# Performance work log

Measured on AMD Instinct MI355X. Metric: run time of the kernel, lower is better.

The kernel has to match this reference:

```python
import jax, jax.numpy as jnp
import numpy as np

N = 50000      # nodes
E = 1600000    # edges (avg degree 32)
F_IN = 128     # num_features
DIM = 64       # hidden dim
L = 3          # num_gc_layers
G = 500        # graphs in batch


def setup_inputs() -> dict:
    key = jax.random.key(0)
    ks = jax.random.split(key, 16)
    inp = {}
    inp["x"] = jax.random.normal(ks[0], (N, F_IN), dtype=jnp.float32)
    inp["edge_index"] = jax.random.randint(ks[1], (2, E), 0, N, dtype=jnp.int32)
    inp["batch"] = jnp.sort(jax.random.randint(ks[2], (N,), 0, G, dtype=jnp.int32))
    # GIN layer MLP params: layer0 maps F_IN->DIM->DIM, later layers DIM->DIM->DIM
    d_in = F_IN
    ki = 3
    for i in range(L):
        inp[f"W1_{i}"] = jax.random.normal(ks[ki], (d_in, DIM), dtype=jnp.float32) / np.sqrt(d_in); ki += 1
        inp[f"b1_{i}"] = jnp.zeros((DIM,), dtype=jnp.float32)
        inp[f"W2_{i}"] = jax.random.normal(ks[ki], (DIM, DIM), dtype=jnp.float32) / np.sqrt(DIM); ki += 1
        inp[f"b2_{i}"] = jnp.zeros((DIM,), dtype=jnp.float32)
        d_in = DIM
    # final scoring head: concat readout -> dim * L inputs, 1 output
    inp["Wm"] = jax.random.normal(ks[ki], (DIM * L, 1), dtype=jnp.float32) / np.sqrt(DIM * L)
    inp["bm"] = jnp.zeros((1,), dtype=jnp.float32)
    return inp


def _segment_softmax(scores, seg, num_segments):
    # numerically stable softmax over elements grouped by seg; scores [M, 1]
    m = jax.ops.segment_max(scores, seg, num_segments=num_segments)
    e = jnp.exp(scores - m[seg])
    denom = jax.ops.segment_sum(e, seg, num_segments=num_segments)
    return e / denom[seg]


def _forward(x, edge_index, batch, params):
    src, dst = edge_index[0], edge_index[1]
    n = x.shape[0]
    xs = []
    h = x
    for i in range(L):
        W1, b1, W2, b2 = params[4 * i: 4 * i + 4]
        # GINConv (eps=0): h_i <- MLP(h_i + sum_{j->i} h_j)
        agg = jax.ops.segment_sum(h[src], dst, num_segments=n)
        h = jax.nn.relu((h + agg) @ W1 + b1) @ W2 + b2
        if i != L - 1:
            h = jax.nn.relu(h)
        xs.append(h)
    node_prob = jnp.concatenate(xs, axis=1)            # concat readout [N, DIM*L]
    Wm, bm = params[4 * L], params[4 * L + 1]
    node_score = node_prob @ Wm + bm                   # [N, 1]
    # lift_node_score_to_edge_score
    src_score = node_score[src]                        # [E, 1]
    dst_score = node_score[dst]
    edge_score = src_score * dst_score
    edge_prop = _segment_softmax(edge_score, dst, n)   # softmax over edges per dst
    new_score = jax.ops.segment_sum(src_score * edge_prop, dst, num_segments=n)
    node_score = node_score + new_score
    # final softmax over nodes grouped by graph id
    return _segment_softmax(node_score, batch, G)


def reference(x, edge_index, batch, W1_0, b1_0, W2_0, b2_0, W1_1, b1_1, W2_1, b2_1,
              W1_2, b1_2, W2_2, b2_2, Wm, bm):
    params = [W1_0, b1_0, W2_0, b2_0, W1_1, b1_1, W2_1, b2_1,
              W1_2, b1_2, W2_2, b2_2, Wm, bm]
    return _forward(x, edge_index, batch, params)
```

## Files before the change

kernel.cpp:

```cpp
#include <hip/hip_runtime.h>
#include <math.h>

#define N_NODES 50000
#define N_EDGES 1600000
#define N_GRAPH 500
#define CHUNKS 64
#define EPC (N_EDGES / CHUNKS)

__device__ __forceinline__ float rl(float v, int k) {
    return __int_as_float(__builtin_amdgcn_readlane(__float_as_int(v), k));
}

__global__ __launch_bounds__(1024) void histsort_kernel(const int* __restrict__ src,
                                                        const int* __restrict__ dst,
                                                        int* __restrict__ csrc_chunk,
                                                        unsigned* __restrict__ cntloc,
                                                        unsigned short* __restrict__ lr_g) {
    __shared__ unsigned packed[N_NODES / 2];
    __shared__ unsigned aux[1024];
    const int c = blockIdx.x;
    const int s0 = c * EPC;
    const int tid = threadIdx.x;

    for (int i = tid; i < N_NODES / 2; i += 1024) packed[i] = 0;
    __syncthreads();

    for (int e = s0 + tid; e < s0 + EPC; e += 1024) {
        int d = dst[e];
        int sh = (d & 1) * 16;
        unsigned old = atomicAdd(&packed[d >> 1], 1u << sh);
        lr_g[e] = (unsigned short)((old >> sh) & 0xffffu);
    }
    __syncthreads();

    const int W = 25;
    int w0 = tid * W;
    int w1 = min(w0 + W, N_NODES / 2);
    unsigned run = 0;
    for (int i = w0; i < w1; i++) {
        unsigned v = packed[i];
        unsigned lo = v & 0xffffu, hi = v >> 16;
        packed[i] = run | ((run + lo) << 16);
        run += lo + hi;
    }
    aux[tid] = run;
    __syncthreads();
    for (int off = 1; off < 1024; off <<= 1) {
        unsigned t = (tid >= off) ? aux[tid - off] : 0;
        __syncthreads();
        aux[tid] += t;
        __syncthreads();
    }
    unsigned b0 = (tid == 0) ? 0 : aux[tid - 1];
    if (b0) {
        unsigned addv = b0 | (b0 << 16);
        for (int i = w0; i < w1; i++) packed[i] += addv;
    }
    __syncthreads();

    int* outc = csrc_chunk + (size_t)c * EPC;
    for (int e = s0 + tid; e < s0 + EPC; e += 1024) {
        int d = dst[e];
        unsigned pw = packed[d >> 1];
        unsigned loc = (d & 1) ? (pw >> 16) : (pw & 0xffffu);
        outc[loc + lr_g[e]] = src[e];
    }
    unsigned* clc = cntloc + (size_t)c * N_NODES;
    for (int d = tid; d < N_NODES; d += 1024) {
        unsigned pw = packed[d >> 1];
        unsigned loc = (d & 1) ? (pw >> 16) : (pw & 0xffffu);
        unsigned nxt;
        if (d + 1 < N_NODES) {
            unsigned pw2 = packed[(d + 1) >> 1];
            nxt = ((d + 1) & 1) ? (pw2 >> 16) : (pw2 & 0xffffu);
        } else {
            nxt = EPC;
        }
        clc[d] = ((nxt - loc) << 16) | loc;
    }
}

__global__ __launch_bounds__(1024) void base_scan1_kernel(const unsigned* __restrict__ cntloc,
                                                          unsigned short* __restrict__ base,
                                                          int* __restrict__ deg,
                                                          int* __restrict__ part, int N) {
    int d = blockIdx.x * 1024 + threadIdx.x;
    int run = 0;
    if (d < N) {
#pragma unroll 8
        for (int c = 0; c < CHUNKS; c++) {
            int v = (int)(cntloc[(size_t)c * N + d] >> 16);
            base[(size_t)c * N + d] = (unsigned short)run;
            run += v;
        }
        deg[d] = run;
    }
    int v = run;
#pragma unroll
    for (int o = 32; o >= 1; o >>= 1) v += __shfl_xor(v, o);
    __shared__ int red[16];
    if ((threadIdx.x & 63) == 0) red[threadIdx.x >> 6] = v;
    __syncthreads();
    if (threadIdx.x == 0) {
        int s = 0;
#pragma unroll
        for (int k = 0; k < 16; k++) s += red[k];
        part[blockIdx.x] = s;
    }
}

__global__ void scan2_kernel(int* __restrict__ part, int nb) {
    int lane = threadIdx.x;
    int v = (lane < nb) ? part[lane] : 0;
    int orig = v;
#pragma unroll
    for (int o = 1; o < 64; o <<= 1) {
        int t = __shfl_up(v, o);
        if (lane >= o) v += t;
    }
    if (lane < nb) part[lane] = v - orig;
    if (lane == nb - 1) part[nb] = v;
}

__global__ __launch_bounds__(1024) void scan3_kernel(const int* __restrict__ deg,
                                                     const int* __restrict__ part,
                                                     int* __restrict__ rowptr, int N) {
    int i = blockIdx.x * 1024 + threadIdx.x;
    int lane = threadIdx.x & 63;
    int w = threadIdx.x >> 6;
    int v = (i < N) ? deg[i] : 0;
    int inc = v;
#pragma unroll
    for (int o = 1; o < 64; o <<= 1) {
        int t = __shfl_up(inc, o);
        if (lane >= o) inc += t;
    }
    __shared__ int wsum[16];
    if (lane == 63) wsum[w] = inc;
    __syncthreads();
    if (threadIdx.x < 16) {
        int x = wsum[threadIdx.x];
        int xo = x;
#pragma unroll
        for (int o = 1; o < 16; o <<= 1) {
            int t = __shfl_up(x, o);
            if ((int)threadIdx.x >= o) x += t;
        }
        wsum[threadIdx.x] = x - xo;
    }
    __syncthreads();
    int b = part[blockIdx.x] + wsum[w];
    if (i < N) {
        rowptr[i] = b + inc - v;
        if (i == N - 1) rowptr[N] = b + inc;
    }
}

__global__ __launch_bounds__(256) void gatherfill_kernel(const int* __restrict__ csrc_chunk,
                                                         const unsigned* __restrict__ cntloc,
                                                         const unsigned short* __restrict__ base,
                                                         const int* __restrict__ rowptr,
                                                         int* __restrict__ csr_src) {
    const int perXcd = N_NODES / 8;
    int xcd = blockIdx.x & 7;
    int idx = (blockIdx.x >> 3) * 4 + ((threadIdx.x) >> 6);
    if (idx >= perXcd) return;
    int wid = xcd * perXcd + idx;
    int lane = threadIdx.x & 63;
    unsigned cl = cntloc[(size_t)lane * N_NODES + wid];
    int cnt = (int)(cl >> 16);
    int loc = (int)(cl & 0xffffu);
    int ob = rowptr[wid] + (int)base[(size_t)lane * N_NODES + wid];
    const int* in = csrc_chunk + (size_t)lane * EPC + loc;
    for (int i = 0; i < cnt; i++) csr_src[ob + i] = in[i];
}

__global__ __launch_bounds__(256) void agg_kernel(const float* __restrict__ y,
                                                  const int* __restrict__ rowptr,
                                                  const int* __restrict__ csr_src,
                                                  float* __restrict__ u, int N) {
    int wid = (blockIdx.x * 256 + threadIdx.x) >> 6;
    int lane = threadIdx.x & 63;
    if (wid >= N) return;
    int q = lane >> 4;
    int r = lane & 15;
    int start = rowptr[wid];
    int end = rowptr[wid + 1];
    float4 acc = make_float4(0.f, 0.f, 0.f, 0.f);
    int j = start;
    for (; j + 32 <= end; j += 32) {
        int s0 = csr_src[j + q];
        int s1 = csr_src[j + 4 + q];
        int s2 = csr_src[j + 8 + q];
        int s3 = csr_src[j + 12 + q];
        int s4 = csr_src[j + 16 + q];
        int s5 = csr_src[j + 20 + q];
        int s6 = csr_src[j + 24 + q];
        int s7 = csr_src[j + 28 + q];
        float4 v0 = *(const float4*)(y + (size_t)s0 * 64 + r * 4);
        float4 v1 = *(const float4*)(y + (size_t)s1 * 64 + r * 4);
        float4 v2 = *(const float4*)(y + (size_t)s2 * 64 + r * 4);
        float4 v3 = *(const float4*)(y + (size_t)s3 * 64 + r * 4);
        float4 v4 = *(const float4*)(y + (size_t)s4 * 64 + r * 4);
        float4 v5 = *(const float4*)(y + (size_t)s5 * 64 + r * 4);
        float4 v6 = *(const float4*)(y + (size_t)s6 * 64 + r * 4);
        float4 v7 = *(const float4*)(y + (size_t)s7 * 64 + r * 4);
        acc.x += ((v0.x + v1.x) + (v2.x + v3.x)) + ((v4.x + v5.x) + (v6.x + v7.x));
        acc.y += ((v0.y + v1.y) + (v2.y + v3.y)) + ((v4.y + v5.y) + (v6.y + v7.y));
        acc.z += ((v0.z + v1.z) + (v2.z + v3.z)) + ((v4.z + v5.z) + (v6.z + v7.z));
        acc.w += ((v0.w + v1.w) + (v2.w + v3.w)) + ((v4.w + v5.w) + (v6.w + v7.w));
    }
#pragma unroll
    for (int m = 0; m < 8; m++) {
        int e = j + 4 * m + q;
        if (e < end) {
            int s = csr_src[e];
            float4 v = *(const float4*)(y + (size_t)s * 64 + r * 4);
            acc.x += v.x; acc.y += v.y; acc.z += v.z; acc.w += v.w;
        }
    }
    acc.x += __shfl_xor(acc.x, 16);
    acc.y += __shfl_xor(acc.y, 16);
    acc.z += __shfl_xor(acc.z, 16);
    acc.w += __shfl_xor(acc.w, 16);
    acc.x += __shfl_xor(acc.x, 32);
    acc.y += __shfl_xor(acc.y, 32);
    acc.z += __shfl_xor(acc.z, 32);
    acc.w += __shfl_xor(acc.w, 32);
    if (lane < 16) {
        float4 self = *(const float4*)(y + (size_t)wid * 64 + r * 4);
        acc.x += self.x; acc.y += self.y; acc.z += self.z; acc.w += self.w;
        *(float4*)(u + (size_t)wid * 64 + r * 4) = acc;
    }
}

__global__ __launch_bounds__(256) void gemm0_kernel(const float* __restrict__ x,
                                                    const float* __restrict__ W1,
                                                    float* __restrict__ y0,
                                                    int N, int totalWaves) {
    int lane = threadIdx.x & 63;
    int wid = (blockIdx.x * 256 + threadIdx.x) >> 6;
    float w[64];
#pragma unroll
    for (int k = 0; k < 64; k++) w[k] = W1[k * 64 + lane];
    for (int node = wid; node < N; node += totalWaves) {
        float xa = x[node * 128 + lane];
        float a0 = 0.f, a1 = 0.f, a2 = 0.f, a3 = 0.f;
#pragma unroll
        for (int k = 0; k < 64; k += 4) {
            a0 = fmaf(rl(xa, k + 0), w[k + 0], a0);
            a1 = fmaf(rl(xa, k + 1), w[k + 1], a1);
            a2 = fmaf(rl(xa, k + 2), w[k + 2], a2);
            a3 = fmaf(rl(xa, k + 3), w[k + 3], a3);
        }
        y0[node * 64 + lane] = (a0 + a1) + (a2 + a3);
    }
#pragma unroll
    for (int k = 0; k < 64; k++) w[k] = W1[(64 + k) * 64 + lane];
    for (int node = wid; node < N; node += totalWaves) {
        float xb = x[node * 128 + 64 + lane];
        float a0 = 0.f, a1 = 0.f, a2 = 0.f, a3 = 0.f;
#pragma unroll
        for (int k = 0; k < 64; k += 4) {
            a0 = fmaf(rl(xb, k + 0), w[k + 0], a0);
            a1 = fmaf(rl(xb, k + 1), w[k + 1], a1);
            a2 = fmaf(rl(xb, k + 2), w[k + 2], a2);
            a3 = fmaf(rl(xb, k + 3), w[k + 3], a3);
        }
        y0[node * 64 + lane] += (a0 + a1) + (a2 + a3);
    }
}

template <int LAYER>
__global__ __launch_bounds__(256) void mlpAB_kernel(const float* __restrict__ u,
                                                    const float* __restrict__ b1,
                                                    const float* __restrict__ W2,
                                                    const float* __restrict__ b2,
                                                    const float* __restrict__ W1n,
                                                    const float* __restrict__ Wm,
                                                    float* __restrict__ ynext,
                                                    float* __restrict__ score,
                                                    int N, int totalWaves) {
    int lane = threadIdx.x & 63;
    int wid = (blockIdx.x * 256 + threadIdx.x) >> 6;
    float w2[64], w1[64];
#pragma unroll
    for (int k = 0; k < 64; k++) w2[k] = W2[k * 64 + lane];
#pragma unroll
    for (int k = 0; k < 64; k++) w1[k] = W1n[k * 64 + lane];
    float bb1 = b1[lane], bb2 = b2[lane], wm = Wm[LAYER * 64 + lane];

    int node = wid;
    float uin = (node < N) ? u[node * 64 + lane] : 0.f;
    for (; node < N; node += totalWaves) {
        int nn = node + totalWaves;
        float unext = (nn < N) ? u[nn * 64 + lane] : 0.f;
        float t = fmaxf(uin + bb1, 0.f);
        float a0 = 0.f, a1 = 0.f, a2 = 0.f, a3 = 0.f;
#pragma unroll
        for (int k = 0; k < 64; k += 4) {
            a0 = fmaf(rl(t, k + 0), w2[k + 0], a0);
            a1 = fmaf(rl(t, k + 1), w2[k + 1], a1);
            a2 = fmaf(rl(t, k + 2), w2[k + 2], a2);
            a3 = fmaf(rl(t, k + 3), w2[k + 3], a3);
        }
        float h = fmaxf(bb2 + ((a0 + a1) + (a2 + a3)), 0.f);
        float p = h * wm;
#pragma unroll
        for (int o = 32; o >= 1; o >>= 1) p += __shfl_xor(p, o);
        if (lane == 0) {
            if (LAYER == 0) score[node] = p;
            else score[node] += p;
        }
        float y0 = 0.f, y1 = 0.f, y2 = 0.f, y3 = 0.f;
#pragma unroll
        for (int k = 0; k < 64; k += 4) {
            y0 = fmaf(rl(h, k + 0), w1[k + 0], y0);
            y1 = fmaf(rl(h, k + 1), w1[k + 1], y1);
            y2 = fmaf(rl(h, k + 2), w1[k + 2], y2);
            y3 = fmaf(rl(h, k + 3), w1[k + 3], y3);
        }
        ynext[node * 64 + lane] = (y0 + y1) + (y2 + y3);
        uin = unext;
    }
}

__global__ __launch_bounds__(256) void mlpA2_kernel(const float* __restrict__ u,
                                                    const float* __restrict__ b1,
                                                    const float* __restrict__ W2,
                                                    const float* __restrict__ b2,
                                                    const float* __restrict__ Wm,
                                                    float* __restrict__ score,
                                                    int N, int totalWaves) {
    int lane = threadIdx.x & 63;
    int wid = (blockIdx.x * 256 + threadIdx.x) >> 6;
    float w2[64];
#pragma unroll
    for (int k = 0; k < 64; k++) w2[k] = W2[k * 64 + lane];
    float bb1 = b1[lane], bb2 = b2[lane], wm = Wm[2 * 64 + lane];

    int node = wid;
    float uin = (node < N) ? u[node * 64 + lane] : 0.f;
    for (; node < N; node += totalWaves) {
        int nn = node + totalWaves;
        float unext = (nn < N) ? u[nn * 64 + lane] : 0.f;
        float t = fmaxf(uin + bb1, 0.f);
        float a0 = 0.f, a1 = 0.f, a2 = 0.f, a3 = 0.f;
#pragma unroll
        for (int k = 0; k < 64; k += 4) {
            a0 = fmaf(rl(t, k + 0), w2[k + 0], a0);
            a1 = fmaf(rl(t, k + 1), w2[k + 1], a1);
            a2 = fmaf(rl(t, k + 2), w2[k + 2], a2);
            a3 = fmaf(rl(t, k + 3), w2[k + 3], a3);
        }
        float h = bb2 + ((a0 + a1) + (a2 + a3));
        float p = h * wm;
#pragma unroll
        for (int o = 32; o >= 1; o >>= 1) p += __shfl_xor(p, o);
        if (lane == 0) score[node] += p;
        uin = unext;
    }
}

__global__ __launch_bounds__(256) void edge_softmax_kernel(const float* __restrict__ score,
                                                           const int* __restrict__ rowptr,
                                                           const int* __restrict__ csr_src,
                                                           const float* __restrict__ bm,
                                                           float* __restrict__ nsf, int N) {
    int wid = (blockIdx.x * blockDim.x + threadIdx.x) >> 6;
    int lane = threadIdx.x & 63;
    if (wid >= N) return;
    float b = bm[0];
    float sd = score[wid] + b;
    int start = rowptr[wid];
    int end = rowptr[wid + 1];
    bool has0 = (start + lane < end);
    float ss0 = 0.f;
    float m = -INFINITY;
    if (has0) {
        ss0 = score[csr_src[start + lane]] + b;
        m = ss0 * sd;
    }
    for (int j = start + 64 + lane; j < end; j += 64) {
        float ss = score[csr_src[j]] + b;
        m = fmaxf(m, ss * sd);
    }
#pragma unroll
    for (int o = 32; o >= 1; o >>= 1) m = fmaxf(m, __shfl_xor(m, o));
    float se = 0.f, swe = 0.f;
    if (m > -INFINITY) {
        if (has0) {
            float e0 = expf(ss0 * sd - m);
            se += e0;
            swe += ss0 * e0;
        }
        for (int j = start + 64 + lane; j < end; j += 64) {
            float ss = score[csr_src[j]] + b;
            float e = expf(ss * sd - m);
            se += e;
            swe += ss * e;
        }
#pragma unroll
        for (int o = 32; o >= 1; o >>= 1) {
            se += __shfl_xor(se, o);
            swe += __shfl_xor(swe, o);
        }
    }
    float ns = (se > 0.f) ? (swe / se) : 0.f;
    if (lane == 0) nsf[wid] = sd + ns;
}

__global__ __launch_bounds__(256) void graph_softmax_kernel(const float* __restrict__ nsf,
                                                            const int* __restrict__ batch,
                                                            float* __restrict__ out, int N) {
    int g = blockIdx.x;
    int tid = threadIdx.x;
    int lo = 0, hi = N;
    while (lo < hi) { int mid = (lo + hi) >> 1; if (batch[mid] < g) lo = mid + 1; else hi = mid; }
    int s0 = lo;
    hi = N;
    while (lo < hi) { int mid = (lo + hi) >> 1; if (batch[mid] < g + 1) lo = mid + 1; else hi = mid; }
    int s1 = lo;

    __shared__ float red[4];
    __shared__ float bval;
    float m = -INFINITY;
    for (int i = s0 + tid; i < s1; i += 256) m = fmaxf(m, nsf[i]);
#pragma unroll
    for (int o = 32; o >= 1; o >>= 1) m = fmaxf(m, __shfl_xor(m, o));
    if ((tid & 63) == 0) red[tid >> 6] = m;
    __syncthreads();
    if (tid == 0) bval = fmaxf(fmaxf(red[0], red[1]), fmaxf(red[2], red[3]));
    __syncthreads();
    float bmx = bval;
    float s = 0.f;
    for (int i = s0 + tid; i < s1; i += 256) {
        float e = expf(nsf[i] - bmx);
        out[i] = e;
        s += e;
    }
#pragma unroll
    for (int o = 32; o >= 1; o >>= 1) s += __shfl_xor(s, o);
    __syncthreads();
    if ((tid & 63) == 0) red[tid >> 6] = s;
    __syncthreads();
    if (tid == 0) bval = red[0] + red[1] + red[2] + red[3];
    __syncthreads();
    float inv = 1.f / bval;
    for (int i = s0 + tid; i < s1; i += 256) out[i] *= inv;
}

extern "C" void kernel_launch(void* const* d_in, const int* in_sizes, int n_in,
                              void* d_out, int out_size, void* d_ws, size_t ws_size,
                              hipStream_t stream) {
    const int N = N_NODES, E = N_EDGES;

    const float* x = (const float*)d_in[0];
    const int* ei = (const int*)d_in[1];
    const int* batch = (const int*)d_in[2];
    const float* W1a[3] = {(const float*)d_in[3], (const float*)d_in[7], (const float*)d_in[11]};
    const float* b1a[3] = {(const float*)d_in[4], (const float*)d_in[8], (const float*)d_in[12]};
    const float* W2a[3] = {(const float*)d_in[5], (const float*)d_in[9], (const float*)d_in[13]};
    const float* b2a[3] = {(const float*)d_in[6], (const float*)d_in[10], (const float*)d_in[14]};
    const float* Wm = (const float*)d_in[15];
    const float* bm = (const float*)d_in[16];
    float* out = (float*)d_out;

    const int* srcp = ei;
    const int* dstp = ei + E;

    float* yA = (float*)d_ws;
    float* yB = yA + (size_t)N * 64;
    float* ubuf = yB + (size_t)N * 64;
    int* csrc_chunk = (int*)ubuf;
    float* score = ubuf + (size_t)N * 64;
    float* nsf = score + N;
    int* deg = (int*)(nsf + N);
    int* rowptr = deg + N;
    int* part = rowptr + N + 1;
    int* csr_src = part + 64;
    unsigned* cntloc = (unsigned*)(csr_src + E);
    unsigned short* base = (unsigned short*)(cntloc + (size_t)CHUNKS * N);
    unsigned short* lr = base + (size_t)CHUNKS * N;

    histsort_kernel<<<CHUNKS, 1024, 0, stream>>>(srcp, dstp, csrc_chunk, cntloc, lr);

    const int nbScan = (N + 1023) / 1024;
    base_scan1_kernel<<<nbScan, 1024, 0, stream>>>(cntloc, base, deg, part, N);
    scan2_kernel<<<1, 64, 0, stream>>>(part, nbScan);
    scan3_kernel<<<nbScan, 1024, 0, stream>>>(deg, part, rowptr, N);

    const int gfBlocks = 8 * ((N / 8 + 3) / 4);
    gatherfill_kernel<<<gfBlocks, 256, 0, stream>>>(csrc_chunk, cntloc, base, rowptr, csr_src);

    const int gw = 4096;
    gemm0_kernel<<<1024, 256, 0, stream>>>(x, W1a[0], yA, N, gw);

    int aggBlocks = (N + 3) / 4;

    agg_kernel<<<aggBlocks, 256, 0, stream>>>(yA, rowptr, csr_src, ubuf, N);
    mlpAB_kernel<0><<<1024, 256, 0, stream>>>(ubuf, b1a[0], W2a[0], b2a[0], W1a[1], Wm, yB, score, N, gw);

    agg_kernel<<<aggBlocks, 256, 0, stream>>>(yB, rowptr, csr_src, ubuf, N);
    mlpAB_kernel<1><<<1024, 256, 0, stream>>>(ubuf, b1a[1], W2a[1], b2a[1], W1a[2], Wm, yA, score, N, gw);

    agg_kernel<<<aggBlocks, 256, 0, stream>>>(yA, rowptr, csr_src, ubuf, N);
    mlpA2_kernel<<<1024, 256, 0, stream>>>(ubuf, b1a[2], W2a[2], b2a[2], Wm, score, N, gw);

    edge_softmax_kernel<<<(N + 3) / 4, 256, 0, stream>>>(score, rowptr, csr_src, bm, nsf, N);

    graph_softmax_kernel<<<N_GRAPH, 256, 0, stream>>>(nsf, batch, out, N);
}
```

Measured before the change: 374.1 us.

## Store node features as fp16, double sort chunks, keep edge ranks in registers

Node feature buffers feeding the neighbour aggregation are now stored in half precision, which halves the bytes of the random gathers, and the sums are still accumulated in fp32. The histogram sort now uses 128 chunks instead of 64. It keeps per-edge local ranks in registers instead of a global array and stores only 16-bit chunk offsets, deriving counts from the difference of adjacent offsets. gemm0 now does both K-halves in one pass with 128 weight registers. The fp16 storage adds rounding error, and the register use in gemm0 may lower occupancy.

```diff
diff --git a/kernel.cpp b/kernel.cpp
--- a/kernel.cpp
+++ b/kernel.cpp
@@ -1,21 +1,30 @@
 #include <hip/hip_runtime.h>
+#include <hip/hip_fp16.h>
 #include <math.h>
 
 #define N_NODES 50000
 #define N_EDGES 1600000
 #define N_GRAPH 500
-#define CHUNKS 64
+#define CHUNKS 128
 #define EPC (N_EDGES / CHUNKS)
+#define NP1 (N_NODES + 1)
+#define NIT ((EPC + 1023) / 1024)
 
 __device__ __forceinline__ float rl(float v, int k) {
     return __int_as_float(__builtin_amdgcn_readlane(__float_as_int(v), k));
+}
+__device__ __forceinline__ void hacc(float4& a, uint2 w) {
+    __half2 h01 = *reinterpret_cast<__half2*>(&w.x);
+    __half2 h23 = *reinterpret_cast<__half2*>(&w.y);
+    float2 f01 = __half22float2(h01);
+    float2 f23 = __half22float2(h23);
+    a.x += f01.x; a.y += f01.y; a.z += f23.x; a.w += f23.y;
 }
 
 __global__ __launch_bounds__(1024) void histsort_kernel(const int* __restrict__ src,
                                                         const int* __restrict__ dst,
                                                         int* __restrict__ csrc_chunk,
-                                                        unsigned* __restrict__ cntloc,
-                                                        unsigned short* __restrict__ lr_g) {
+                                                        unsigned short* __restrict__ locs) {
     __shared__ unsigned packed[N_NODES / 2];
     __shared__ unsigned aux[1024];
     const int c = blockIdx.x;
@@ -25,11 +34,16 @@
     for (int i = tid; i < N_NODES / 2; i += 1024) packed[i] = 0;
     __syncthreads();
 
-    for (int e = s0 + tid; e < s0 + EPC; e += 1024) {
-        int d = dst[e];
-        int sh = (d & 1) * 16;
-        unsigned old = atomicAdd(&packed[d >> 1], 1u << sh);
-        lr_g[e] = (unsigned short)((old >> sh) & 0xffffu);
+    unsigned short lrv[NIT];
+#pragma unroll
+    for (int it = 0; it < NIT; it++) {
+        int e = s0 + it * 1024 + tid;
+        if (e < s0 + EPC) {
+            int d = dst[e];
+            int sh = (d & 1) * 16;
+            unsigned old = atomicAdd(&packed[d >> 1], 1u << sh);
+            lrv[it] = (unsigned short)((old >> sh) & 0xffffu);
+        }
     }
     __syncthreads();
 
@@ -59,28 +73,30 @@
     __syncthreads();
 
     int* outc = csrc_chunk + (size_t)c * EPC;
-    for (int e = s0 + tid; e < s0 + EPC; e += 1024) {
-        int d = dst[e];
-        unsigned pw = packed[d >> 1];
-        unsigned loc = (d & 1) ? (pw >> 16) : (pw & 0xffffu);
-        outc[loc + lr_g[e]] = src[e];
-    }
-    unsigned* clc = cntloc + (size_t)c * N_NODES;
-    for (int d = tid; d < N_NODES; d += 1024) {
-        unsigned pw = packed[d >> 1];
-        unsigned loc = (d & 1) ? (pw >> 16) : (pw & 0xffffu);
-        unsigned nxt;
-        if (d + 1 < N_NODES) {
-            unsigned pw2 = packed[(d + 1) >> 1];
-            nxt = ((d + 1) & 1) ? (pw2 >> 16) : (pw2 & 0xffffu);
+#pragma unroll
+    for (int it = 0; it < NIT; it++) {
+        int e = s0 + it * 1024 + tid;
+        if (e < s0 + EPC) {
+            int d = dst[e];
+            unsigned pw = packed[d >> 1];
+            unsigned loc = (d & 1) ? (pw >> 16) : (pw & 0xffffu);
+            outc[loc + lrv[it]] = src[e];
+        }
+    }
+    unsigned short* lc = locs + (size_t)c * NP1;
+    for (int d = tid; d <= N_NODES; d += 1024) {
+        unsigned short loc;
+        if (d == N_NODES) {
+            loc = (unsigned short)EPC;
         } else {
-            nxt = EPC;
-        }
-        clc[d] = ((nxt - loc) << 16) | loc;
-    }
-}
-
-__global__ __launch_bounds__(1024) void base_scan1_kernel(const unsigned* __restrict__ cntloc,
+            unsigned pw = packed[d >> 1];
+            loc = (unsigned short)((d & 1) ? (pw >> 16) : (pw & 0xffffu));
+        }
+        lc[d] = loc;
+    }
+}
+
+__global__ __launch_bounds__(1024) void base_scan1_kernel(const unsigned short* __restrict__ locs,
                                                           unsigned short* __restrict__ base,
                                                           int* __restrict__ deg,
                                                           int* __restrict__ part, int N) {
@@ -89,9 +105,10 @@
     if (d < N) {
 #pragma unroll 8
         for (int c = 0; c < CHUNKS; c++) {
-            int v = (int)(cntloc[(size_t)c * N + d] >> 16);
+            int l0 = locs[(size_t)c * NP1 + d];
+            int l1 = locs[(size_t)c * NP1 + d + 1];
             base[(size_t)c * N + d] = (unsigned short)run;
-            run += v;
+            run += l1 - l0;
         }
         deg[d] = run;
     }
@@ -157,25 +174,31 @@
 }
 
 __global__ __launch_bounds__(256) void gatherfill_kernel(const int* __restrict__ csrc_chunk,
-                                                         const unsigned* __restrict__ cntloc,
+                                                         const unsigned short* __restrict__ locs,
                                                          const unsigned short* __restrict__ base,
                                                          const int* __restrict__ rowptr,
                                                          int* __restrict__ csr_src) {
     const int perXcd = N_NODES / 8;
     int xcd = blockIdx.x & 7;
-    int idx = (blockIdx.x >> 3) * 4 + ((threadIdx.x) >> 6);
+    int idx = (blockIdx.x >> 3) * 4 + (threadIdx.x >> 6);
     if (idx >= perXcd) return;
     int wid = xcd * perXcd + idx;
     int lane = threadIdx.x & 63;
-    unsigned cl = cntloc[(size_t)lane * N_NODES + wid];
-    int cnt = (int)(cl >> 16);
-    int loc = (int)(cl & 0xffffu);
-    int ob = rowptr[wid] + (int)base[(size_t)lane * N_NODES + wid];
-    const int* in = csrc_chunk + (size_t)lane * EPC + loc;
-    for (int i = 0; i < cnt; i++) csr_src[ob + i] = in[i];
-}
-
-__global__ __launch_bounds__(256) void agg_kernel(const float* __restrict__ y,
+    int rp = rowptr[wid];
+#pragma unroll
+    for (int cc = 0; cc < 2; cc++) {
+        int c = lane + cc * 64;
+        const unsigned short* lc = locs + (size_t)c * NP1;
+        int l0 = lc[wid];
+        int l1 = lc[wid + 1];
+        int cnt = l1 - l0;
+        int ob = rp + (int)base[(size_t)c * N_NODES + wid];
+        const int* in = csrc_chunk + (size_t)c * EPC + l0;
+        for (int i = 0; i < cnt; i++) csr_src[ob + i] = in[i];
+    }
+}
+
+__global__ __launch_bounds__(256) void agg_kernel(const __half* __restrict__ yh,
                                                   const int* __restrict__ rowptr,
                                                   const int* __restrict__ csr_src,
                                                   float* __restrict__ u, int N) {
@@ -197,26 +220,24 @@
         int s5 = csr_src[j + 20 + q];
         int s6 = csr_src[j + 24 + q];
         int s7 = csr_src[j + 28 + q];
-        float4 v0 = *(const float4*)(y + (size_t)s0 * 64 + r * 4);
-        float4 v1 = *(const float4*)(y + (size_t)s1 * 64 + r * 4);
-        float4 v2 = *(const float4*)(y + (size_t)s2 * 64 + r * 4);
-        float4 v3 = *(const float4*)(y + (size_t)s3 * 64 + r * 4);
-        float4 v4 = *(const float4*)(y + (size_t)s4 * 64 + r * 4);
-        float4 v5 = *(const float4*)(y + (size_t)s5 * 64 + r * 4);
-        float4 v6 = *(const float4*)(y + (size_t)s6 * 64 + r * 4);
-        float4 v7 = *(const float4*)(y + (size_t)s7 * 64 + r * 4);
-        acc.x += ((v0.x + v1.x) + (v2.x + v3.x)) + ((v4.x + v5.x) + (v6.x + v7.x));
-        acc.y += ((v0.y + v1.y) + (v2.y + v3.y)) + ((v4.y + v5.y) + (v6.y + v7.y));
-        acc.z += ((v0.z + v1.z) + (v2.z + v3.z)) + ((v4.z + v5.z) + (v6.z + v7.z));
-        acc.w += ((v0.w + v1.w) + (v2.w + v3.w)) + ((v4.w + v5.w) + (v6.w + v7.w));
+        uint2 w0 = *(const uint2*)(yh + (size_t)s0 * 64 + r * 4);
+        uint2 w1 = *(const uint2*)(yh + (size_t)s1 * 64 + r * 4);
+        uint2 w2 = *(const uint2*)(yh + (size_t)s2 * 64 + r * 4);
+        uint2 w3 = *(const uint2*)(yh + (size_t)s3 * 64 + r * 4);
+        uint2 w4 = *(const uint2*)(yh + (size_t)s4 * 64 + r * 4);
+        uint2 w5 = *(const uint2*)(yh + (size_t)s5 * 64 + r * 4);
+        uint2 w6 = *(const uint2*)(yh + (size_t)s6 * 64 + r * 4);
+        uint2 w7 = *(const uint2*)(yh + (size_t)s7 * 64 + r * 4);
+        hacc(acc, w0); hacc(acc, w1); hacc(acc, w2); hacc(acc, w3);
+        hacc(acc, w4); hacc(acc, w5); hacc(acc, w6); hacc(acc, w7);
     }
 #pragma unroll
     for (int m = 0; m < 8; m++) {
         int e = j + 4 * m + q;
         if (e < end) {
             int s = csr_src[e];
-            float4 v = *(const float4*)(y + (size_t)s * 64 + r * 4);
-            acc.x += v.x; acc.y += v.y; acc.z += v.z; acc.w += v.w;
+            uint2 w = *(const uint2*)(yh + (size_t)s * 64 + r * 4);
+            hacc(acc, w);
         }
     }
     acc.x += __shfl_xor(acc.x, 16);
@@ -228,46 +249,42 @@
     acc.z += __shfl_xor(acc.z, 32);
     acc.w += __shfl_xor(acc.w, 32);
     if (lane < 16) {
-        float4 self = *(const float4*)(y + (size_t)wid * 64 + r * 4);
-        acc.x += self.x; acc.y += self.y; acc.z += self.z; acc.w += self.w;
+        uint2 w = *(const uint2*)(yh + (size_t)wid * 64 + r * 4);
+        hacc(acc, w);
         *(float4*)(u + (size_t)wid * 64 + r * 4) = acc;
     }
 }
 
 __global__ __launch_bounds__(256) void gemm0_kernel(const float* __restrict__ x,
                                                     const float* __restrict__ W1,
-                                                    float* __restrict__ y0,
+                                                    __half* __restrict__ y0,
                                                     int N, int totalWaves) {
     int lane = threadIdx.x & 63;
     int wid = (blockIdx.x * 256 + threadIdx.x) >> 6;
-    float w[64];
-#pragma unroll
-    for (int k = 0; k < 64; k++) w[k] = W1[k * 64 + lane];
+    float wA[64], wB[64];
+#pragma unroll
+    for (int k = 0; k < 64; k++) wA[k] = W1[k * 64 + lane];
+#pragma unroll
+    for (int k = 0; k < 64; k++) wB[k] = W1[(64 + k) * 64 + lane];
     for (int node = wid; node < N; node += totalWaves) {
-        float xa = x[node * 128 + lane];
+        float xa = x[(size_t)node * 128 + lane];
+        float xb = x[(size_t)node * 128 + 64 + lane];
         float a0 = 0.f, a1 = 0.f, a2 = 0.f, a3 = 0.f;
 #pragma unroll
         for (int k = 0; k < 64; k += 4) {
-            a0 = fmaf(rl(xa, k + 0), w[k + 0], a0);
-            a1 = fmaf(rl(xa, k + 1), w[k + 1], a1);
-            a2 = fmaf(rl(xa, k + 2), w[k + 2], a2);
-            a3 = fmaf(rl(xa, k + 3), w[k + 3], a3);
-        }
-        y0[node * 64 + lane] = (a0 + a1) + (a2 + a3);
-    }
-#pragma unroll
-    for (int k = 0; k < 64; k++) w[k] = W1[(64 + k) * 64 + lane];
-    for (int node = wid; node < N; node += totalWaves) {
-        float xb = x[node * 128 + 64 + lane];
-        float a0 = 0.f, a1 = 0.f, a2 = 0.f, a3 = 0.f;
+            a0 = fmaf(rl(xa, k + 0), wA[k + 0], a0);
+            a1 = fmaf(rl(xa, k + 1), wA[k + 1], a1);
+            a2 = fmaf(rl(xa, k + 2), wA[k + 2], a2);
+            a3 = fmaf(rl(xa, k + 3), wA[k + 3], a3);
+        }
 #pragma unroll
         for (int k = 0; k < 64; k += 4) {
-            a0 = fmaf(rl(xb, k + 0), w[k + 0], a0);
-            a1 = fmaf(rl(xb, k + 1), w[k + 1], a1);
-            a2 = fmaf(rl(xb, k + 2), w[k + 2], a2);
-            a3 = fmaf(rl(xb, k + 3), w[k + 3], a3);
-        }
-        y0[node * 64 + lane] += (a0 + a1) + (a2 + a3);
+            a0 = fmaf(rl(xb, k + 0), wB[k + 0], a0);
+            a1 = fmaf(rl(xb, k + 1), wB[k + 1], a1);
+            a2 = fmaf(rl(xb, k + 2), wB[k + 2], a2);
+            a3 = fmaf(rl(xb, k + 3), wB[k + 3], a3);
+        }
+        y0[(size_t)node * 64 + lane] = __float2half((a0 + a1) + (a2 + a3));
     }
 }
 
@@ -278,7 +295,7 @@
                                                     const float* __restrict__ b2,
                                                     const float* __restrict__ W1n,
                                                     const float* __restrict__ Wm,
-                                                    float* __restrict__ ynext,
+                                                    __half* __restrict__ ynext,
                                                     float* __restrict__ score,
                                                     int N, int totalWaves) {
     int lane = threadIdx.x & 63;
@@ -291,10 +308,10 @@
     float bb1 = b1[lane], bb2 = b2[lane], wm = Wm[LAYER * 64 + lane];
 
     int node = wid;
-    float uin = (node < N) ? u[node * 64 + lane] : 0.f;
+    float uin = (node < N) ? u[(size_t)node * 64 + lane] : 0.f;
     for (; node < N; node += totalWaves) {
         int nn = node + totalWaves;
-        float unext = (nn < N) ? u[nn * 64 + lane] : 0.f;
+        float unext = (nn < N) ? u[(size_t)nn * 64 + lane] : 0.f;
         float t = fmaxf(uin + bb1, 0.f);
         float a0 = 0.f, a1 = 0.f, a2 = 0.f, a3 = 0.f;
 #pragma unroll
@@ -320,7 +337,7 @@
             y2 = fmaf(rl(h, k + 2), w1[k + 2], y2);
             y3 = fmaf(rl(h, k + 3), w1[k + 3], y3);
         }
-        ynext[node * 64 + lane] = (y0 + y1) + (y2 + y3);
+        ynext[(size_t)node * 64 + lane] = __float2half((y0 + y1) + (y2 + y3));
         uin = unext;
     }
 }
@@ -340,10 +357,10 @@
     float bb1 = b1[lane], bb2 = b2[lane], wm = Wm[2 * 64 + lane];
 
     int node = wid;
-    float uin = (node < N) ? u[node * 64 + lane] : 0.f;
+    float uin = (node < N) ? u[(size_t)node * 64 + lane] : 0.f;
     for (; node < N; node += totalWaves) {
         int nn = node + totalWaves;
-        float unext = (nn < N) ? u[nn * 64 + lane] : 0.f;
+        float unext = (nn < N) ? u[(size_t)nn * 64 + lane] : 0.f;
         float t = fmaxf(uin + bb1, 0.f);
         float a0 = 0.f, a1 = 0.f, a2 = 0.f, a3 = 0.f;
 #pragma unroll
@@ -469,29 +486,28 @@
     const int* srcp = ei;
     const int* dstp = ei + E;
 
-    float* yA = (float*)d_ws;
-    float* yB = yA + (size_t)N * 64;
-    float* ubuf = yB + (size_t)N * 64;
+    float* ubuf = (float*)d_ws;
     int* csrc_chunk = (int*)ubuf;
-    float* score = ubuf + (size_t)N * 64;
+    __half* yA = (__half*)(ubuf + (size_t)N * 64);
+    __half* yB = yA + (size_t)N * 64;
+    float* score = (float*)(yB + (size_t)N * 64);
     float* nsf = score + N;
     int* deg = (int*)(nsf + N);
     int* rowptr = deg + N;
     int* part = rowptr + N + 1;
     int* csr_src = part + 64;
-    unsigned* cntloc = (unsigned*)(csr_src + E);
-    unsigned short* base = (unsigned short*)(cntloc + (size_t)CHUNKS * N);
-    unsigned short* lr = base + (size_t)CHUNKS * N;
-
-    histsort_kernel<<<CHUNKS, 1024, 0, stream>>>(srcp, dstp, csrc_chunk, cntloc, lr);
+    unsigned short* locs = (unsigned short*)(csr_src + E);
+    unsigned short* base = locs + (size_t)CHUNKS * NP1;
+
+    histsort_kernel<<<CHUNKS, 1024, 0, stream>>>(srcp, dstp, csrc_chunk, locs);
 
     const int nbScan = (N + 1023) / 1024;
-    base_scan1_kernel<<<nbScan, 1024, 0, stream>>>(cntloc, base, deg, part, N);
+    base_scan1_kernel<<<nbScan, 1024, 0, stream>>>(locs, base, deg, part, N);
     scan2_kernel<<<1, 64, 0, stream>>>(part, nbScan);
     scan3_kernel<<<nbScan, 1024, 0, stream>>>(deg, part, rowptr, N);
 
     const int gfBlocks = 8 * ((N / 8 + 3) / 4);
-    gatherfill_kernel<<<gfBlocks, 256, 0, stream>>>(csrc_chunk, cntloc, base, rowptr, csr_src);
+    gatherfill_kernel<<<gfBlocks, 256, 0, stream>>>(csrc_chunk, locs, base, rowptr, csr_src);
 
     const int gw = 4096;
     gemm0_kernel<<<1024, 256, 0, stream>>>(x, W1a[0], yA, N, gw);
```

New measurement: 339.4 us. 1.1x faster.
